# Performance work log

Hardware: AMD Instinct MI355X
Metric: run time of the kernel (lower is better)

The kernel has to match this reference:

```python
import jax, jax.numpy as jnp
import numpy as np

B, S, D, SIZE = 32, 2048, 1024, 1024

def setup_inputs() -> dict:
    key = jax.random.key(0)
    k1, k2, k3, k4, k5 = jax.random.split(key, 5)
    return {
        "inputs": jax.random.normal(k1, (B, S, D), dtype=jnp.float32),
        "g": jax.random.normal(k2, (B, D), dtype=jnp.float32),
        "WO": jax.random.normal(k3, (SIZE, D), dtype=jnp.float32) * 0.05,
        "WG": jax.random.normal(k4, (SIZE, D), dtype=jnp.float32) * 0.05,
        "v": jax.random.normal(k5, (1, SIZE), dtype=jnp.float32) * 0.05,
    }

def reference(inputs, g, WO, WG, v):
    # term1[b,s,k] = WO @ inputs[b,s]; term2[b,k] = WG @ g[b]
    term1 = jnp.einsum('kd,bsd->bsk', WO, inputs)
    term2 = jnp.einsum('kd,bd->bk', WG, g)
    tan_sum = jnp.tanh(term1 + term2[:, None, :])  # [B,S,SIZE]
    # final[b,s] = v @ tan_sum[b,s]  (v is [1,SIZE]); squeeze -> [B,S]
    return jnp.einsum('k,bsk->bs', v[0], tan_sum)
```

## Files before the change

### kernel.cpp

```cpp
#include <hip/hip_runtime.h>
#include <hip/hip_bf16.h>

#define BB   32
#define SS   2048
#define DD   1024
#define SZ   1024
#define MM   (BB*SS)

typedef short bf16x8 __attribute__((ext_vector_type(8)));
typedef float f32x4  __attribute__((ext_vector_type(4)));

__device__ __forceinline__ unsigned short f2bf(float x) {
    unsigned u = __float_as_uint(x);
    u += 0x7fffu + ((u >> 16) & 1u);
    return (unsigned short)(u >> 16);
}
__device__ __forceinline__ unsigned pack2_bf16(float a, float b) {
    return (unsigned)f2bf(a) | ((unsigned)f2bf(b) << 16);
}

__device__ __forceinline__ float ftanh(float x) {
    float e = __expf(2.0f * x);
    return 1.0f - 2.0f / (e + 1.0f);
}

__global__ void prep_kernel(const float* __restrict__ WO,
                            const float* __restrict__ WG,
                            const float* __restrict__ g,
                            unsigned short* __restrict__ WOb,
                            float* __restrict__ term2) {
    __shared__ float gs[DD];
    int bid = blockIdx.x, tid = threadIdx.x;
    if (bid < 1024) {
        int base = bid * 1024 + tid * 4;
        float4 w = *(const float4*)(WO + base);
        unsigned p0 = pack2_bf16(w.x, w.y), p1 = pack2_bf16(w.z, w.w);
        *(uint2*)&WOb[base] = make_uint2(p0, p1);
    } else {
        int id = bid - 1024;
        int b  = id >> 2;
        int k  = ((id & 3) << 8) + tid;
        #pragma unroll
        for (int r = 0; r < 4; r++) gs[r * 256 + tid] = g[b * DD + r * 256 + tid];
        __syncthreads();
        const float* wr = WG + (size_t)k * DD;
        float s = 0.f;
        #pragma unroll 4
        for (int d = 0; d < DD; d += 4) {
            float4 wv = *(const float4*)(wr + d);
            s += wv.x * gs[d] + wv.y * gs[d + 1] + wv.z * gs[d + 2] + wv.w * gs[d + 3];
        }
        term2[b * SZ + k] = s;
    }
}

__global__ __launch_bounds__(256, 2) void fused_main(
    const float* __restrict__ Ain,
    const unsigned short* __restrict__ WOb,
    const float* __restrict__ term2,
    const float* __restrict__ v,
    float* __restrict__ out) {
    __shared__ unsigned short Asm[128 * 40];
    __shared__ unsigned short Bsm[256 * 32];
    __shared__ float part[2][128];

    const int tid  = threadIdx.x;
    const int wave = tid >> 6;
    const int lane = tid & 63;
    const int wm = wave & 1, wn = wave >> 1;
    const int l15 = lane & 15;
    const int k8  = lane >> 4;

    const int bid   = blockIdx.x;
    const int ntile = bid & 3;
    const int mtile = bid >> 2;
    const int m0 = mtile * 128;
    const int n0 = ntile * 256;
    const int bidx = m0 >> 11;

    f32x4 acc[4][8];
    #pragma unroll
    for (int i = 0; i < 4; i++)
        #pragma unroll
        for (int j = 0; j < 8; j++) acc[i][j] = (f32x4){0.f, 0.f, 0.f, 0.f};

    for (int k0 = 0; k0 < DD; k0 += 32) {
        #pragma unroll
        for (int r = 0; r < 4; r++) {
            int chunk = r * 256 + tid;
            int n = chunk >> 2, ks = chunk & 3;
            const unsigned short* src = WOb + (size_t)(n0 + n) * DD + k0 + ks * 8;
            __builtin_amdgcn_global_load_lds(
                (const __attribute__((address_space(1))) void*)src,
                (__attribute__((address_space(3))) void*)(&Bsm[chunk * 8]),
                16, 0, 0);
        }
        #pragma unroll
        for (int r = 0; r < 4; r++) {
            int e = r * 256 + tid;
            int row = e >> 3, qc = e & 7;
            float4 av = *(const float4*)(Ain + (size_t)(m0 + row) * DD + k0 + qc * 4);
            unsigned p0 = pack2_bf16(av.x, av.y), p1 = pack2_bf16(av.z, av.w);
            *(uint2*)&Asm[row * 40 + qc * 4] = make_uint2(p0, p1);
        }
        __syncthreads();

        bf16x8 afr[4], bfr[8];
        #pragma unroll
        for (int mi = 0; mi < 4; mi++)
            afr[mi] = *(const bf16x8*)&Asm[(wm * 64 + mi * 16 + l15) * 40 + k8 * 8];
        #pragma unroll
        for (int ni = 0; ni < 8; ni++)
            bfr[ni] = *(const bf16x8*)&Bsm[(wn * 128 + ni * 16 + l15) * 32 + k8 * 8];
        #pragma unroll
        for (int ni = 0; ni < 8; ni++)
            #pragma unroll
            for (int mi = 0; mi < 4; mi++)
                acc[mi][ni] = __builtin_amdgcn_mfma_f32_16x16x32_bf16(
                    afr[mi], bfr[ni], acc[mi][ni], 0, 0, 0);
        __syncthreads();
    }

    float rsum[4][4];
    #pragma unroll
    for (int mi = 0; mi < 4; mi++)
        #pragma unroll
        for (int r = 0; r < 4; r++) rsum[mi][r] = 0.f;

    #pragma unroll
    for (int ni = 0; ni < 8; ni++) {
        int gn = n0 + wn * 128 + ni * 16 + l15;
        float t2 = term2[bidx * SZ + gn];
        float vv = v[gn];
        #pragma unroll
        for (int mi = 0; mi < 4; mi++)
            #pragma unroll
            for (int r = 0; r < 4; r++)
                rsum[mi][r] += ftanh(acc[mi][ni][r] + t2) * vv;
    }
    #pragma unroll
    for (int mi = 0; mi < 4; mi++)
        #pragma unroll
        for (int r = 0; r < 4; r++) {
            float s = rsum[mi][r];
            s += __shfl_xor(s, 1, 16);
            s += __shfl_xor(s, 2, 16);
            s += __shfl_xor(s, 4, 16);
            s += __shfl_xor(s, 8, 16);
            rsum[mi][r] = s;
        }
    float val = 0.f;
    #pragma unroll
    for (int mi = 0; mi < 4; mi++)
        #pragma unroll
        for (int r = 0; r < 4; r++)
            if (l15 == mi * 4 + r) val = rsum[mi][r];
    {
        int mi = l15 >> 2, r = l15 & 3;
        part[wn][wm * 64 + mi * 16 + k8 * 4 + r] = val;
    }
    __syncthreads();
    if (tid < 128) atomicAdd(&out[m0 + tid], part[0][tid] + part[1][tid]);
}

extern "C" void kernel_launch(void* const* d_in, const int* in_sizes, int n_in,
                              void* d_out, int out_size, void* d_ws, size_t ws_size,
                              hipStream_t stream) {
    const float* inputs = (const float*)d_in[0];
    const float* g      = (const float*)d_in[1];
    const float* WO     = (const float*)d_in[2];
    const float* WG     = (const float*)d_in[3];
    const float* v      = (const float*)d_in[4];
    float* out = (float*)d_out;

    unsigned short* WOb = (unsigned short*)d_ws;
    float* term2 = (float*)((char*)d_ws + (size_t)SZ * DD * 2);

    (void)hipMemsetAsync(d_out, 0, sizeof(float) * MM, stream);
    prep_kernel<<<1024 + 128, 256, 0, stream>>>(WO, WG, g, WOb, term2);
    fused_main<<<(MM / 128) * (SZ / 256), 256, 0, stream>>>(inputs, WOb, term2, v, out);
}
```

Measured before the change: 571.0 us.

## Double-buffer GEMM main loop with pre-swizzled WO layout and block remap

Changes the bf16 WO copy into a k-group-major layout so each B tile stages with contiguous 16-byte global_load_lds copies. The fused kernel now double-buffers A and B in LDS: it prefetches the next A slice into registers and issues the next B async copy while running MFMAs on the current buffer, which leaves one barrier per iteration. Block IDs are also remapped so blocks sharing an M tile are spread across XCDs, and MFMA issue priority is raised with s_setprio. LDS use doubles and the register count for A prefetch rises, which may affect occupancy at 2 blocks per CU.

```diff
diff --git a/kernel.cpp b/kernel.cpp
--- a/kernel.cpp
+++ b/kernel.cpp
@@ -32,10 +32,12 @@
     __shared__ float gs[DD];
     int bid = blockIdx.x, tid = threadIdx.x;
     if (bid < 1024) {
-        int base = bid * 1024 + tid * 4;
-        float4 w = *(const float4*)(WO + base);
+        int q = bid;
+        int d = tid * 4;
+        float4 w = *(const float4*)(WO + (size_t)q * DD + d);
         unsigned p0 = pack2_bf16(w.x, w.y), p1 = pack2_bf16(w.z, w.w);
-        *(uint2*)&WOb[base] = make_uint2(p0, p1);
+        int dst = ((d >> 5) * 4096 + ((d >> 3) & 3) * 1024 + q) * 8 + (d & 7);
+        *(uint2*)&WOb[dst] = make_uint2(p0, p1);
     } else {
         int id = bid - 1024;
         int b  = id >> 2;
@@ -60,66 +62,99 @@
     const float* __restrict__ term2,
     const float* __restrict__ v,
     float* __restrict__ out) {
-    __shared__ unsigned short Asm[128 * 40];
-    __shared__ unsigned short Bsm[256 * 32];
+    __shared__ unsigned short Asm[2 * 4096];
+    __shared__ unsigned short Bsm[2 * 8192];
     __shared__ float part[2][128];
 
     const int tid  = threadIdx.x;
     const int wave = tid >> 6;
     const int lane = tid & 63;
-    const int wm = wave & 1, wn = wave >> 1;
+    const int wm  = wave & 1, wn = wave >> 1;
     const int l15 = lane & 15;
-    const int k8  = lane >> 4;
-
-    const int bid   = blockIdx.x;
-    const int ntile = bid & 3;
-    const int mtile = bid >> 2;
+    const int kgl = lane >> 4;
+
+    const int bid     = blockIdx.x;
+    const int logical = (bid & 7) * 256 + (bid >> 3);
+    const int ntile = logical & 3;
+    const int mtile = logical >> 2;
     const int m0 = mtile * 128;
     const int n0 = ntile * 256;
     const int bidx = m0 >> 11;
 
+    const int rowb = tid >> 3;
+    const int sub  = tid & 7;
+    const int kgA  = sub >> 1, halfA = sub & 1;
+
     f32x4 acc[4][8];
     #pragma unroll
     for (int i = 0; i < 4; i++)
         #pragma unroll
         for (int j = 0; j < 8; j++) acc[i][j] = (f32x4){0.f, 0.f, 0.f, 0.f};
 
-    for (int k0 = 0; k0 < DD; k0 += 32) {
-        #pragma unroll
-        for (int r = 0; r < 4; r++) {
-            int chunk = r * 256 + tid;
-            int n = chunk >> 2, ks = chunk & 3;
-            const unsigned short* src = WOb + (size_t)(n0 + n) * DD + k0 + ks * 8;
+    float4 areg[4];
+
+    auto LOAD_A = [&](int k0) {
+        #pragma unroll
+        for (int r = 0; r < 4; r++) {
+            int row = r * 32 + rowb;
+            areg[r] = *(const float4*)(Ain + (size_t)(m0 + row) * DD + k0 + sub * 4);
+        }
+    };
+    auto WRITE_A = [&](int buf) {
+        #pragma unroll
+        for (int r = 0; r < 4; r++) {
+            int row = r * 32 + rowb;
+            unsigned p0 = pack2_bf16(areg[r].x, areg[r].y);
+            unsigned p1 = pack2_bf16(areg[r].z, areg[r].w);
+            *(uint2*)&Asm[buf * 4096 + (kgA * 128 + row) * 8 + halfA * 4] =
+                make_uint2(p0, p1);
+        }
+    };
+    auto STAGE_B = [&](int buf, int k0) {
+        const int dstep = k0 >> 5;
+        #pragma unroll
+        for (int r = 0; r < 4; r++) {
+            const unsigned short* src = WOb + dstep * 32768 + r * 8192 + (n0 + tid) * 8;
             __builtin_amdgcn_global_load_lds(
                 (const __attribute__((address_space(1))) void*)src,
-                (__attribute__((address_space(3))) void*)(&Bsm[chunk * 8]),
+                (__attribute__((address_space(3))) void*)(&Bsm[buf * 8192 + (r * 256 + tid) * 8]),
                 16, 0, 0);
         }
-        #pragma unroll
-        for (int r = 0; r < 4; r++) {
-            int e = r * 256 + tid;
-            int row = e >> 3, qc = e & 7;
-            float4 av = *(const float4*)(Ain + (size_t)(m0 + row) * DD + k0 + qc * 4);
-            unsigned p0 = pack2_bf16(av.x, av.y), p1 = pack2_bf16(av.z, av.w);
-            *(uint2*)&Asm[row * 40 + qc * 4] = make_uint2(p0, p1);
-        }
-        __syncthreads();
-
+    };
+    auto COMPUTE = [&](int buf) {
         bf16x8 afr[4], bfr[8];
+        const int aoff = (kgl * 128 + wm * 64 + l15) * 8;
+        const int boff = (kgl * 256 + wn * 128 + l15) * 8;
         #pragma unroll
         for (int mi = 0; mi < 4; mi++)
-            afr[mi] = *(const bf16x8*)&Asm[(wm * 64 + mi * 16 + l15) * 40 + k8 * 8];
+            afr[mi] = *(const bf16x8*)&Asm[buf * 4096 + aoff + mi * 128];
         #pragma unroll
         for (int ni = 0; ni < 8; ni++)
-            bfr[ni] = *(const bf16x8*)&Bsm[(wn * 128 + ni * 16 + l15) * 32 + k8 * 8];
+            bfr[ni] = *(const bf16x8*)&Bsm[buf * 8192 + boff + ni * 128];
+        __builtin_amdgcn_s_setprio(1);
         #pragma unroll
         for (int ni = 0; ni < 8; ni++)
             #pragma unroll
             for (int mi = 0; mi < 4; mi++)
                 acc[mi][ni] = __builtin_amdgcn_mfma_f32_16x16x32_bf16(
                     afr[mi], bfr[ni], acc[mi][ni], 0, 0, 0);
+        __builtin_amdgcn_s_setprio(0);
+    };
+
+    LOAD_A(0);
+    STAGE_B(0, 0);
+    WRITE_A(0);
+    __syncthreads();
+
+    for (int t = 0; t < 31; ++t) {
+        const int cur = t & 1;
+        LOAD_A((t + 1) << 5);
+        STAGE_B(cur ^ 1, (t + 1) << 5);
+        COMPUTE(cur);
+        WRITE_A(cur ^ 1);
         __syncthreads();
     }
+    COMPUTE(1);
 
     float rsum[4][4];
     #pragma unroll
@@ -157,7 +192,7 @@
             if (l15 == mi * 4 + r) val = rsum[mi][r];
     {
         int mi = l15 >> 2, r = l15 & 3;
-        part[wn][wm * 64 + mi * 16 + k8 * 4 + r] = val;
+        part[wn][wm * 64 + mi * 16 + kgl * 4 + r] = val;
     }
     __syncthreads();
     if (tid < 128) atomicAdd(&out[m0 + tid], part[0][tid] + part[1][tid]);
```

Result: no change. 575.0 us (+0.7%).
